# Optimization experiments

Measured on AMD Instinct MI355X. Metric: run time of the kernel, lower is better.

Reference implementation:

```python
import jax, jax.numpy as jnp
import numpy as np

B, S, D, H = 256, 64, 1024, 16
DH = D // H          # 64
BOARD = 8
NREL = 2 * (BOARD - 1) + 1  # 15


def _rel_indices():
    # Relative row/col offsets between all pairs of board squares, shifted to [0, 2*(BOARD-1)]
    coords = np.arange(S)
    row = coords // BOARD
    col = coords % BOARD
    rr = row[:, None] - row[None, :] + (BOARD - 1)  # (S, S)
    rc = col[:, None] - col[None, :] + (BOARD - 1)  # (S, S)
    return jnp.asarray(rr), jnp.asarray(rc)


def setup_inputs() -> dict:
    key = jax.random.key(0)
    ks = jax.random.split(key, 12)
    p = lambda k, sh: jax.random.normal(k, sh, jnp.float32) * 0.02
    return {
        "x": jax.random.normal(ks[0], (B, S, D), jnp.float32),
        "wq": p(ks[1], (D, D)),
        "wk": p(ks[2], (D, D)),
        "wv": p(ks[3], (D, D)),
        "wo": p(ks[4], (D, D)),
        "bo": jnp.zeros((D,), jnp.float32),
        "eq_h": p(ks[5], (NREL, DH)),
        "eq_w": p(ks[6], (NREL, DH)),
        "ek_h": p(ks[7], (NREL, DH)),
        "ek_w": p(ks[8], (NREL, DH)),
        "ev_h": p(ks[9], (NREL, DH)),
        "ev_w": p(ks[10], (NREL, DH)),
    }


def reference(x, wq, wk, wv, wo, bo, eq_h, eq_w, ek_h, ek_w, ev_h, ev_w):
    rr, rc = _rel_indices()
    rel_q = eq_h[rr] + eq_w[rc]  # (S, S, DH)
    rel_k = ek_h[rr] + ek_w[rc]
    rel_v = ev_h[rr] + ev_w[rc]

    def heads(y):
        return y.reshape(B, S, H, DH).transpose(0, 2, 1, 3)  # (B, H, S, DH)

    q = heads(x @ wq.T)
    k = heads(x @ wk.T)
    v = heads(x @ wv.T)

    # (q_i + rq_ij) . (k_j + rk_ij), expanded to avoid the (B,H,S,S,DH) intermediates
    scores = (
        jnp.einsum('bhid,bhjd->bhij', q, k)
        + jnp.einsum('bhid,ijd->bhij', q, rel_k)
        + jnp.einsum('ijd,bhjd->bhij', rel_q, k)
        + jnp.sum(rel_q * rel_k, axis=-1)[None, None]
    )
    attn = jax.nn.softmax(scores / jnp.sqrt(jnp.float32(DH)), axis=-1)  # (B, H, S, S)

    # sum_j attn_ij * (v_j + rv_ij)
    ctx = (
        jnp.einsum('bhij,bhjd->bhid', attn, v)
        + jnp.einsum('bhij,ijd->bhid', attn, rel_v)
    )
    ctx = ctx.transpose(0, 2, 1, 3).reshape(B, S, D)
    return ctx @ wo.T + bo
```

## Files before the change

kernel.cpp:

```cpp
#include <hip/hip_runtime.h>
#include <hip/hip_bf16.h>

typedef __hip_bfloat16 bf16;
typedef __attribute__((ext_vector_type(8))) short short8;
typedef __attribute__((ext_vector_type(8))) unsigned short ushort8;
typedef __attribute__((ext_vector_type(4))) float floatx4;

__device__ __forceinline__ short f2s(float x) {
  bf16 h = __float2bfloat16(x);
  short s;
  __builtin_memcpy(&s, &h, 2);
  return s;
}

__device__ __forceinline__ void gl_lds16(const bf16* g, bf16* l) {
  __builtin_amdgcn_global_load_lds(
      (const __attribute__((address_space(1))) unsigned int*)g,
      (__attribute__((address_space(3))) unsigned int*)l, 16, 0, 0);
}

#define MFMA16(a, b, c) __builtin_amdgcn_mfma_f32_16x16x32_bf16((a), (b), (c), 0, 0, 0)

__global__ __launch_bounds__(256) void convert_f32_bf16(
    const float* __restrict__ src, bf16* __restrict__ dst, int n) {
  const int i = (blockIdx.x * 256 + threadIdx.x) * 8;
  if (i + 7 < n) {
    float4 a = *(const float4*)(src + i);
    float4 b = *(const float4*)(src + i + 4);
    short8 r;
    r[0] = f2s(a.x); r[1] = f2s(a.y); r[2] = f2s(a.z); r[3] = f2s(a.w);
    r[4] = f2s(b.x); r[5] = f2s(b.y); r[6] = f2s(b.z); r[7] = f2s(b.w);
    *(short8*)(dst + i) = r;
  }
}

__global__ __launch_bounds__(256) void precompute_tables(
    const float* __restrict__ eqh, const float* __restrict__ eqw,
    const float* __restrict__ ekh, const float* __restrict__ ekw,
    const float* __restrict__ evh, const float* __restrict__ evw,
    bf16* __restrict__ ews, float* __restrict__ S4f)
{
  const int t = threadIdx.x;
  if (t < 96) {
    const int tb = t >> 4, row = t & 15;
    const float* src[6] = {eqh, eqw, ekh, ekw, evh, evw};
    bf16* dst = ews + tb * 1024 + row * 64;
    if (row < 15) {
      const float* s = src[tb] + row * 64;
      #pragma unroll
      for (int d = 0; d < 64; d += 8) {
        float4 a = *(const float4*)(s + d);
        float4 b2 = *(const float4*)(s + d + 4);
        short8 rr;
        rr[0] = f2s(a.x); rr[1] = f2s(a.y); rr[2] = f2s(a.z); rr[3] = f2s(a.w);
        rr[4] = f2s(b2.x); rr[5] = f2s(b2.y); rr[6] = f2s(b2.z); rr[7] = f2s(b2.w);
        *(short8*)(dst + d) = rr;
      }
    } else {
      const short8 z = {0, 0, 0, 0, 0, 0, 0, 0};
      #pragma unroll
      for (int d = 0; d < 64; d += 8) *(short8*)(dst + d) = z;
    }
  }
  if (t < 225) {
    const int r = t / 15, c = t % 15;
    float s = 0.f;
    for (int d = 0; d < 64; ++d)
      s += (eqh[r * 64 + d] + eqw[c * 64 + d]) * (ekh[r * 64 + d] + ekw[c * 64 + d]);
    S4f[t] = s;
  }
}

template <int TAG>
__global__ __launch_bounds__(256) void gemm_bt(
    const bf16* __restrict__ A,
    const void* __restrict__ W0, const void* __restrict__ W1, const void* __restrict__ W2,
    int wBf,
    const float* __restrict__ bias, int hasBias,
    bf16* __restrict__ O0, bf16* __restrict__ O1, bf16* __restrict__ O2,
    float* __restrict__ Ofp, int outF32)
{
  __shared__ bf16 As[128 * 64];
  __shared__ bf16 Bs[128 * 64];

  const int m0 = blockIdx.x * 128;
  const int by = blockIdx.y;
  const int which = by >> 3;
  const void* W = (which == 0) ? W0 : (which == 1) ? W1 : W2;
  bf16* O = (which == 0) ? O0 : (which == 1) ? O1 : O2;
  const int n0 = (by & 7) * 128;

  const int t = threadIdx.x;
  const int lane = t & 63, w = t >> 6;
  const int lrow = lane >> 3, lcol = (lane & 7) * 8;
  const int wm = w >> 1, wn = w & 1;
  const int quad = lane >> 4, n16 = lane & 15;

  const int swzA = ((lrow & 1) << 5) | (((lrow >> 1) & 3) << 3);
  const int gcol = lcol ^ swzA;
  const int swzR = ((n16 & 1) << 5) | (((n16 >> 1) & 3) << 3);

  floatx4 acc[4][4];
  const floatx4 zero4 = {0.f, 0.f, 0.f, 0.f};
  #pragma unroll
  for (int mi = 0; mi < 4; ++mi)
    #pragma unroll
    for (int ni = 0; ni < 4; ++ni) acc[mi][ni] = zero4;

  const int arowb = m0 + w * 32 + lrow;
  const int browb = n0 + w * 32 + lrow;
  bf16* lau = As + w * 2048;
  bf16* lbu = Bs + w * 2048;

  if (wBf) {
    const bf16* Wb = (const bf16*)W;
    for (int k0 = 0; k0 < 1024; k0 += 64) {
      if (k0) __syncthreads();
      const bf16* ga = A + arowb * 1024 + k0 + gcol;
      const bf16* gw = Wb + browb * 1024 + k0 + gcol;
      #pragma unroll
      for (int c = 0; c < 4; ++c) {
        gl_lds16(ga + c * 8192, lau + c * 512);
        gl_lds16(gw + c * 8192, lbu + c * 512);
      }
      __syncthreads();
      #pragma unroll
      for (int ks = 0; ks < 2; ++ks) {
        short8 af[4], bfv[4];
        #pragma unroll
        for (int mi = 0; mi < 4; ++mi)
          af[mi] = *(const short8*)(As + (wm * 64 + mi * 16 + n16) * 64 +
                                    ((ks * 32 + quad * 8) ^ swzR));
        #pragma unroll
        for (int ni = 0; ni < 4; ++ni)
          bfv[ni] = *(const short8*)(Bs + (wn * 64 + ni * 16 + n16) * 64 +
                                     ((ks * 32 + quad * 8) ^ swzR));
        #pragma unroll
        for (int mi = 0; mi < 4; ++mi)
          #pragma unroll
          for (int ni = 0; ni < 4; ++ni)
            acc[mi][ni] = MFMA16(af[mi], bfv[ni], acc[mi][ni]);
      }
    }
  } else {
    const float* Wf = (const float*)W;
    for (int k0 = 0; k0 < 1024; k0 += 64) {
      short8 rb[4];
      #pragma unroll
      for (int c = 0; c < 4; ++c) {
        const float* f = Wf + (browb + c * 8) * 1024 + k0 + gcol;
        float4 a = *(const float4*)f;
        float4 b = *(const float4*)(f + 4);
        short8 r;
        r[0] = f2s(a.x); r[1] = f2s(a.y); r[2] = f2s(a.z); r[3] = f2s(a.w);
        r[4] = f2s(b.x); r[5] = f2s(b.y); r[6] = f2s(b.z); r[7] = f2s(b.w);
        rb[c] = r;
      }
      if (k0) __syncthreads();
      const bf16* ga = A + arowb * 1024 + k0 + gcol;
      #pragma unroll
      for (int c = 0; c < 4; ++c) {
        gl_lds16(ga + c * 8192, lau + c * 512);
        *(short8*)(lbu + lane * 8 + c * 512) = rb[c];
      }
      __syncthreads();
      #pragma unroll
      for (int ks = 0; ks < 2; ++ks) {
        short8 af[4], bfv[4];
        #pragma unroll
        for (int mi = 0; mi < 4; ++mi)
          af[mi] = *(const short8*)(As + (wm * 64 + mi * 16 + n16) * 64 +
                                    ((ks * 32 + quad * 8) ^ swzR));
        #pragma unroll
        for (int ni = 0; ni < 4; ++ni)
          bfv[ni] = *(const short8*)(Bs + (wn * 64 + ni * 16 + n16) * 64 +
                                     ((ks * 32 + quad * 8) ^ swzR));
        #pragma unroll
        for (int mi = 0; mi < 4; ++mi)
          #pragma unroll
          for (int ni = 0; ni < 4; ++ni)
            acc[mi][ni] = MFMA16(af[mi], bfv[ni], acc[mi][ni]);
      }
    }
  }

  #pragma unroll
  for (int ni = 0; ni < 4; ++ni) {
    const int col = n0 + wn * 64 + ni * 16 + n16;
    const float bv = hasBias ? bias[col] : 0.f;
    #pragma unroll
    for (int mi = 0; mi < 4; ++mi) {
      #pragma unroll
      for (int r = 0; r < 4; ++r) {
        const int row = m0 + wm * 64 + mi * 16 + quad * 4 + r;
        if (outF32) Ofp[row * 1024 + col] = acc[mi][ni][r] + bv;
        else        O[row * 1024 + col] = __float2bfloat16(acc[mi][ni][r] + bv);
      }
    }
  }
}

__global__ __launch_bounds__(256, 3) void attn_rel(
    const bf16* __restrict__ Q, const bf16* __restrict__ Km, const bf16* __restrict__ V,
    const bf16* __restrict__ ews, const float* __restrict__ S4f,
    bf16* __restrict__ Ctx)
{
  __shared__ bf16 vT[64][106];
  __shared__ bf16 pa[64][104];
  __shared__ float Ahs[64][16], Aws[64][16];
  __shared__ float Bhs[15][64], Bws[15][64];
  __shared__ float S4s[225];

  const int t = threadIdx.x;
  const int b = blockIdx.x >> 4, h = blockIdx.x & 15;
  const int base = b * 65536 + h * 64;
  const int lane = t & 63, w = t >> 6;
  const int quad = lane >> 4, n16 = lane & 15;

  const bf16* qrow = Q + base + (w * 16 + n16) * 1024 + quad * 8;
  short8 aq0 = *(const short8*)(qrow);
  short8 aq1 = *(const short8*)(qrow + 32);
  short8 bk0[4], bk1[4];
  #pragma unroll
  for (int nj = 0; nj < 4; ++nj) {
    const bf16* krow = Km + base + (nj * 16 + n16) * 1024 + quad * 8;
    bk0[nj] = *(const short8*)(krow);
    bk1[nj] = *(const short8*)(krow + 32);
  }
  short8 ebf[4][2];
  #pragma unroll
  for (int tb = 0; tb < 4; ++tb) {
    const bf16* er = ews + tb * 1024 + n16 * 64 + quad * 8;
    ebf[tb][0] = *(const short8*)(er);
    ebf[tb][1] = *(const short8*)(er + 32);
  }

  {
    const int r = t >> 2, c0 = (t & 3) * 16;
    const bf16* vrow = V + base + r * 1024 + c0;
    int4 v0 = *(const int4*)(vrow);
    int4 v1 = *(const int4*)(vrow + 8);
    const unsigned short* p0 = (const unsigned short*)&v0;
    const unsigned short* p1 = (const unsigned short*)&v1;
    #pragma unroll
    for (int ii = 0; ii < 8; ++ii) {
      *(unsigned short*)&vT[c0 + ii][r] = p0[ii];
      *(unsigned short*)&vT[c0 + 8 + ii][r] = p1[ii];
    }
    if (t < 60) {
      const int r2 = t >> 2, d0 = (t & 3) * 16;
      ushort8 pe0 = *(const ushort8*)(ews + 4096 + r2 * 64 + d0);
      ushort8 pe1 = *(const ushort8*)(ews + 4096 + r2 * 64 + d0 + 8);
      ushort8 pf0 = *(const ushort8*)(ews + 5120 + r2 * 64 + d0);
      ushort8 pf1 = *(const ushort8*)(ews + 5120 + r2 * 64 + d0 + 8);
      #pragma unroll
      for (int ii = 0; ii < 8; ++ii) {
        *(unsigned short*)&vT[d0 + ii][64 + r2] = pe0[ii];
        *(unsigned short*)&vT[d0 + 8 + ii][64 + r2] = pe1[ii];
        *(unsigned short*)&vT[d0 + ii][79 + r2] = pf0[ii];
        *(unsigned short*)&vT[d0 + 8 + ii][79 + r2] = pf1[ii];
      }
    }
    if (t < 64) {
      *(unsigned short*)&vT[t][94] = 0; *(unsigned short*)&vT[t][95] = 0;
      *(unsigned short*)&pa[t][94] = 0; *(unsigned short*)&pa[t][95] = 0;
    }
    if (t < 225) S4s[t] = S4f[t];
  }

  floatx4 cqk[4];
  #pragma unroll
  for (int nj = 0; nj < 4; ++nj) {
    floatx4 c = {0.f, 0.f, 0.f, 0.f};
    c = MFMA16(aq0, bk0[nj], c);
    c = MFMA16(aq1, bk1[nj], c);
    cqk[nj] = c;
  }
  {
    floatx4 cah = {0.f, 0.f, 0.f, 0.f}, caw = cah, cbh = cah, cbw = cah;
    cah = MFMA16(aq0, ebf[2][0], cah); cah = MFMA16(aq1, ebf[2][1], cah);
    caw = MFMA16(aq0, ebf[3][0], caw); caw = MFMA16(aq1, ebf[3][1], caw);
    cbh = MFMA16(bk0[w], ebf[0][0], cbh); cbh = MFMA16(bk1[w], ebf[0][1], cbh);
    cbw = MFMA16(bk0[w], ebf[1][0], cbw); cbw = MFMA16(bk1[w], ebf[1][1], cbw);
    #pragma unroll
    for (int r = 0; r < 4; ++r) {
      const int i = w * 16 + quad * 4 + r;
      Ahs[i][n16] = cah[r];
      Aws[i][n16] = caw[r];
      if (n16 < 15) { Bhs[n16][i] = cbh[r]; Bws[n16][i] = cbw[r]; }
    }
  }
  __syncthreads();

  const int i_base = w * 16 + quad * 4;
  float xv[4][4];
  #pragma unroll
  for (int nj = 0; nj < 4; ++nj) {
    const int j = nj * 16 + n16;
    const int rowj = j >> 3, colj = j & 7;
    #pragma unroll
    for (int r = 0; r < 4; ++r) {
      const int i = i_base + r;
      const int rowi = i >> 3, coli = i & 7;
      const int rr = rowi - rowj + 7, rc = coli - colj + 7;
      xv[r][nj] = (cqk[nj][r] + Ahs[i][rr] + Aws[i][rc] + Bhs[rr][j] + Bws[rc][j]
                   + S4s[rr * 15 + rc]) * 0.125f;
    }
  }
  #pragma unroll
  for (int r = 0; r < 4; ++r) {
    const int i = i_base + r;
    const int rowi = i >> 3, coli = i & 7;
    float mx = fmaxf(fmaxf(xv[r][0], xv[r][1]), fmaxf(xv[r][2], xv[r][3]));
    #pragma unroll
    for (int off = 1; off < 16; off <<= 1) mx = fmaxf(mx, __shfl_xor(mx, off));
    float p[4];
    float sm = 0.f;
    #pragma unroll
    for (int nj = 0; nj < 4; ++nj) { p[nj] = __expf(xv[r][nj] - mx); sm += p[nj]; }
    #pragma unroll
    for (int off = 1; off < 16; off <<= 1) sm += __shfl_xor(sm, off);
    const float inv = 1.0f / sm;
    #pragma unroll
    for (int nj = 0; nj < 4; ++nj) {
      p[nj] *= inv;
      pa[i][nj * 16 + n16] = __float2bfloat16(p[nj]);
    }
    float ph[4];
    #pragma unroll
    for (int nj = 0; nj < 4; ++nj) {
      float v = p[nj];
      v += __shfl_xor(v, 1); v += __shfl_xor(v, 2); v += __shfl_xor(v, 4);
      ph[nj] = v;
    }
    float s4 = p[0] + p[1] + p[2] + p[3];
    float pw = s4 + __shfl_xor(s4, 8);
    if ((n16 & 7) == 0) {
      const int hh = n16 >> 3;
      #pragma unroll
      for (int nj = 0; nj < 4; ++nj) {
        const int g = nj * 2 + hh;
        pa[i][64 + rowi + 7 - g] = __float2bfloat16(ph[nj]);
      }
    } else if (n16 < 8) {
      const int z = n16 - 1;
      pa[i][64 + (z < rowi ? z : z + 8)] = __float2bfloat16(0.f);
    }
    if (n16 < 8) {
      pa[i][79 + coli + 7 - n16] = __float2bfloat16(pw);
    } else {
      const int z = n16 - 8;
      pa[i][79 + (z < coli ? z : z + 8)] = __float2bfloat16(0.f);
    }
  }
  __threadfence_block();

  short8 ap[3];
  #pragma unroll
  for (int ksb = 0; ksb < 3; ++ksb)
    ap[ksb] = *(const short8*)&pa[w * 16 + n16][ksb * 32 + quad * 8];
  #pragma unroll
  for (int nj = 0; nj < 4; ++nj) {
    floatx4 c = {0.f, 0.f, 0.f, 0.f};
    #pragma unroll
    for (int ksb = 0; ksb < 3; ++ksb) {
      short8 bv = *(const short8*)&vT[nj * 16 + n16][ksb * 32 + quad * 8];
      c = MFMA16(ap[ksb], bv, c);
    }
    #pragma unroll
    for (int r = 0; r < 4; ++r) {
      const int i = i_base + r;
      Ctx[base + i * 1024 + nj * 16 + n16] = __float2bfloat16(c[r]);
    }
  }
}

extern "C" void kernel_launch(void* const* d_in, const int* in_sizes, int n_in,
                              void* d_out, int out_size, void* d_ws, size_t ws_size,
                              hipStream_t stream) {
  const float* x   = (const float*)d_in[0];
  const float* wq  = (const float*)d_in[1];
  const float* wk  = (const float*)d_in[2];
  const float* wv  = (const float*)d_in[3];
  const float* wo  = (const float*)d_in[4];
  const float* bo  = (const float*)d_in[5];
  const float* eqh = (const float*)d_in[6];
  const float* eqw = (const float*)d_in[7];
  const float* ekh = (const float*)d_in[8];
  const float* ekw = (const float*)d_in[9];
  const float* evh = (const float*)d_in[10];
  const float* evw = (const float*)d_in[11];
  float* outf = (float*)d_out;

  const size_t hdr = (ws_size - 16384) & ~(size_t)1023;
  bf16* ewsB = (bf16*)((char*)d_ws + hdr);
  float* S4f = (float*)((char*)d_ws + hdr + 12288);
  precompute_tables<<<1, 256, 0, stream>>>(eqh, eqw, ekh, ekw, evh, evw, ewsB, S4f);

  if (ws_size >= (size_t)73 * 1024 * 1024) {
    bf16* qb = (bf16*)d_ws;
    bf16* kb = qb + 16777216;
    bf16* wqb = kb + 16777216;
    bf16* wkb = wqb + 1048576;
    bf16* wvb = wkb + 1048576;
    bf16* wob = wvb + 1048576;
    bf16* xb = (bf16*)d_out;
    bf16* vb = (bf16*)((char*)d_out + 33554432);

    convert_f32_bf16<<<8192, 256, 0, stream>>>(x, xb, 16777216);
    convert_f32_bf16<<<512, 256, 0, stream>>>(wq, wqb, 1048576);
    convert_f32_bf16<<<512, 256, 0, stream>>>(wk, wkb, 1048576);
    convert_f32_bf16<<<512, 256, 0, stream>>>(wv, wvb, 1048576);
    convert_f32_bf16<<<512, 256, 0, stream>>>(wo, wob, 1048576);

    gemm_bt<0><<<dim3(128, 24), 256, 0, stream>>>(
        xb, wqb, wkb, wvb, 1, nullptr, 0, qb, kb, vb, nullptr, 0);
    attn_rel<<<dim3(4096), 256, 0, stream>>>(qb, kb, vb, ewsB, S4f, qb);
    gemm_bt<1><<<dim3(128, 8), 256, 0, stream>>>(
        qb, wob, nullptr, nullptr, 1, bo, 1, nullptr, nullptr, nullptr, outf, 1);
  } else {
    bf16* xb0 = (bf16*)((char*)d_out + 16777216);
    bf16* xb1 = (bf16*)((char*)d_out + 50331648);
    bf16* vQ2 = (bf16*)((char*)d_out + 33554432);
    bf16* qb = (bf16*)d_ws;
    bf16* kb = qb + 8388608;
    const int fastW = (ws_size >= (size_t)42 * 1024 * 1024) ? 1 : 0;
    bf16* wqb = kb + 8388608;
    bf16* wkb = wqb + 1048576;
    bf16* wvb = wkb + 1048576;
    bf16* wob = wvb + 1048576;

    convert_f32_bf16<<<4096, 256, 0, stream>>>(x, xb0, 8388608);
    convert_f32_bf16<<<4096, 256, 0, stream>>>(x + 8388608, xb1, 8388608);
    if (fastW) {
      convert_f32_bf16<<<512, 256, 0, stream>>>(wq, wqb, 1048576);
      convert_f32_bf16<<<512, 256, 0, stream>>>(wk, wkb, 1048576);
      convert_f32_bf16<<<512, 256, 0, stream>>>(wv, wvb, 1048576);
      convert_f32_bf16<<<512, 256, 0, stream>>>(wo, wob, 1048576);
    }

    for (int hh = 0; hh < 2; ++hh) {
      const bf16* xh = hh ? xb1 : xb0;
      gemm_bt<0><<<dim3(64, 24), 256, 0, stream>>>(
          xh,
          fastW ? (const void*)wqb : (const void*)wq,
          fastW ? (const void*)wkb : (const void*)wk,
          fastW ? (const void*)wvb : (const void*)wv,
          fastW, nullptr, 0, qb, kb, vQ2, nullptr, 0);
      attn_rel<<<dim3(2048), 256, 0, stream>>>(qb, kb, vQ2, ewsB, S4f, qb);
      gemm_bt<1><<<dim3(64, 8), 256, 0, stream>>>(
          qb,
          fastW ? (const void*)wob : (const void*)wo, nullptr, nullptr,
          fastW, bo, 1, nullptr, nullptr, nullptr,
          outf + (size_t)hh * 8388608, 1);
    }
  }
}
```

Measured before the change: 386.4 us.

## Replace projection GEMMs with 256x256-tile, 4-stage pipelined 512-thread kernel

Adds a new gemm256 kernel with 256x256 output tiles, 512 threads, a 4-deep LDS ring filled by direct global-to-LDS loads with explicit vmcnt waits, swizzled LDS layout, an XCD-aware block remap and s_setprio around the MFMA bursts. It replaces gemm_bt for the QKV and output projections wherever bf16 weights are available. The goal is more operand reuse per tile and memory latency hidden behind MFMA work. In exchange it uses 128KB of LDS and many accumulator registers, which limits occupancy and makes the hand-written wait counts fragile.

Result: slower. 394.2 us (+2.0%).

```diff
diff --git a/kernel.cpp b/kernel.cpp
--- a/kernel.cpp
+++ b/kernel.cpp
@@ -20,6 +20,14 @@
 }
 
 #define MFMA16(a, b, c) __builtin_amdgcn_mfma_f32_16x16x32_bf16((a), (b), (c), 0, 0, 0)
+
+__device__ __forceinline__ void bar() {
+  asm volatile("" ::: "memory");
+  __builtin_amdgcn_s_barrier();
+  asm volatile("" ::: "memory");
+}
+
+#define VMCNT(N) asm volatile("s_waitcnt vmcnt(" #N ")" ::: "memory")
 
 __global__ __launch_bounds__(256) void convert_f32_bf16(
     const float* __restrict__ src, bf16* __restrict__ dst, int n) {
@@ -68,6 +76,130 @@
     for (int d = 0; d < 64; ++d)
       s += (eqh[r * 64 + d] + eqw[c * 64 + d]) * (ekh[r * 64 + d] + ekw[c * 64 + d]);
     S4f[t] = s;
+  }
+}
+
+template <int TAG>
+__global__ __launch_bounds__(512, 2) void gemm256(
+    const bf16* __restrict__ A,
+    const bf16* __restrict__ W0, const bf16* __restrict__ W1, const bf16* __restrict__ W2,
+    const float* __restrict__ bias, int hasBias,
+    bf16* __restrict__ O0, bf16* __restrict__ O1, bf16* __restrict__ O2,
+    float* __restrict__ Ofp, int outF32)
+{
+  __shared__ bf16 lds[65536];
+
+  const int nx = gridDim.x;
+  const int nwg = nx * gridDim.y;
+  const int orig = blockIdx.y * nx + blockIdx.x;
+  const int id = (orig & 7) * (nwg >> 3) + (orig >> 3);
+  const int bx = id % nx;
+  const int by = id / nx;
+
+  const int m0 = bx * 256;
+  const int which = by >> 2;
+  const bf16* W = (which == 0) ? W0 : (which == 1) ? W1 : W2;
+  bf16* O = (which == 0) ? O0 : (which == 1) ? O1 : O2;
+  const int n0 = (by & 3) * 256;
+
+  const int t = threadIdx.x;
+  const int lane = t & 63, w = t >> 6;
+  const int wm = w >> 2, wn = w & 3;
+  const int quad = lane >> 4, n16 = lane & 15;
+
+  const int srow = (t >> 6) * 16 + ((t & 63) >> 2);
+  const int scol = ((t & 3) * 8) ^ (((t >> 5) & 1) << 4);
+  const bf16* Abase = A + (m0 + srow) * 1024 + scol;
+  const bf16* Bbase = W + (n0 + srow) * 1024 + scol;
+  const int wdst = w * 512;
+
+  const int swzq = (quad * 8) ^ ((n16 >> 3) << 4);
+  const int aoff = wm * 4096 + n16 * 32 + swzq;
+  const int boff = wn * 2048 + n16 * 32 + swzq;
+
+  floatx4 acc[8][4];
+  const floatx4 zero4 = {0.f, 0.f, 0.f, 0.f};
+  #pragma unroll
+  for (int mi = 0; mi < 8; ++mi)
+    #pragma unroll
+    for (int ni = 0; ni < 4; ++ni) acc[mi][ni] = zero4;
+
+  #pragma unroll
+  for (int p = 0; p < 3; ++p) {
+    const bf16* ga = Abase + p * 32;
+    bf16* la = lds + p * 16384 + wdst;
+    gl_lds16(ga, la); gl_lds16(ga + 131072, la + 4096);
+    const bf16* gb = Bbase + p * 32;
+    bf16* lb = lds + p * 16384 + 8192 + wdst;
+    gl_lds16(gb, lb); gl_lds16(gb + 131072, lb + 4096);
+  }
+  VMCNT(8);
+  bar();
+
+#define TILE_STEP(TT, DOSTAGE, WAITSEQ) do {                                   \
+    const bf16* bA_ = lds + ((TT) & 3) * 16384;                                \
+    const bf16* bB_ = bA_ + 8192;                                              \
+    short8 af_[4], bq_[4];                                                     \
+    _Pragma("unroll")                                                          \
+    for (int mi = 0; mi < 4; ++mi)                                             \
+      af_[mi] = *(const short8*)(bA_ + aoff + mi * 512);                       \
+    _Pragma("unroll")                                                          \
+    for (int ni = 0; ni < 4; ++ni)                                             \
+      bq_[ni] = *(const short8*)(bB_ + boff + ni * 512);                       \
+    if (DOSTAGE) {                                                             \
+      const bf16* g_ = Abase + ((TT) + 3) * 32;                                \
+      bf16* l_ = lds + (((TT) + 3) & 3) * 16384 + wdst;                        \
+      gl_lds16(g_, l_); gl_lds16(g_ + 131072, l_ + 4096);                      \
+    }                                                                          \
+    bar();                                                                     \
+    __builtin_amdgcn_s_setprio(1);                                             \
+    _Pragma("unroll")                                                          \
+    for (int mi = 0; mi < 4; ++mi)                                             \
+      _Pragma("unroll")                                                        \
+      for (int ni = 0; ni < 4; ++ni)                                           \
+        acc[mi][ni] = MFMA16(af_[mi], bq_[ni], acc[mi][ni]);                   \
+    __builtin_amdgcn_s_setprio(0);                                             \
+    _Pragma("unroll")                                                          \
+    for (int mi = 0; mi < 4; ++mi)                                             \
+      af_[mi] = *(const short8*)(bA_ + aoff + 2048 + mi * 512);                \
+    if (DOSTAGE) {                                                             \
+      const bf16* g_ = Bbase + ((TT) + 3) * 32;                                \
+      bf16* l_ = lds + (((TT) + 3) & 3) * 16384 + 8192 + wdst;                 \
+      gl_lds16(g_, l_); gl_lds16(g_ + 131072, l_ + 4096);                      \
+    }                                                                          \
+    bar();                                                                     \
+    __builtin_amdgcn_s_setprio(1);                                             \
+    _Pragma("unroll")                                                          \
+    for (int mi = 0; mi < 4; ++mi)                                             \
+      _Pragma("unroll")                                                        \
+      for (int ni = 0; ni < 4; ++ni)                                           \
+        acc[mi + 4][ni] = MFMA16(af_[mi], bq_[ni], acc[mi + 4][ni]);           \
+    __builtin_amdgcn_s_setprio(0);                                             \
+    WAITSEQ;                                                                   \
+  } while (0)
+
+  #pragma unroll 1
+  for (int tt = 0; tt < 29; ++tt) {
+    TILE_STEP(tt, 1, VMCNT(8); bar());
+  }
+  TILE_STEP(29, 0, VMCNT(4); bar());
+  TILE_STEP(30, 0, VMCNT(0); bar());
+  TILE_STEP(31, 0, (void)0);
+#undef TILE_STEP
+
+  #pragma unroll
+  for (int ni = 0; ni < 4; ++ni) {
+    const int col = n0 + wn * 64 + ni * 16 + n16;
+    const float bv = hasBias ? bias[col] : 0.f;
+    #pragma unroll
+    for (int mi = 0; mi < 8; ++mi) {
+      #pragma unroll
+      for (int r = 0; r < 4; ++r) {
+        const int row = m0 + wm * 128 + mi * 16 + quad * 4 + r;
+        if (outF32) Ofp[row * 1024 + col] = acc[mi][ni][r] + bv;
+        else        O[row * 1024 + col] = __float2bfloat16(acc[mi][ni][r] + bv);
+      }
+    }
   }
 }
 
@@ -413,11 +545,11 @@
     convert_f32_bf16<<<512, 256, 0, stream>>>(wv, wvb, 1048576);
     convert_f32_bf16<<<512, 256, 0, stream>>>(wo, wob, 1048576);
 
-    gemm_bt<0><<<dim3(128, 24), 256, 0, stream>>>(
-        xb, wqb, wkb, wvb, 1, nullptr, 0, qb, kb, vb, nullptr, 0);
+    gemm256<0><<<dim3(64, 12), 512, 0, stream>>>(
+        xb, wqb, wkb, wvb, nullptr, 0, qb, kb, vb, nullptr, 0);
     attn_rel<<<dim3(4096), 256, 0, stream>>>(qb, kb, vb, ewsB, S4f, qb);
-    gemm_bt<1><<<dim3(128, 8), 256, 0, stream>>>(
-        qb, wob, nullptr, nullptr, 1, bo, 1, nullptr, nullptr, nullptr, outf, 1);
+    gemm256<1><<<dim3(64, 4), 512, 0, stream>>>(
+        qb, wob, nullptr, nullptr, bo, 1, nullptr, nullptr, nullptr, outf, 1);
   } else {
     bf16* xb0 = (bf16*)((char*)d_out + 16777216);
     bf16* xb1 = (bf16*)((char*)d_out + 50331648);
@@ -441,18 +573,25 @@
 
     for (int hh = 0; hh < 2; ++hh) {
       const bf16* xh = hh ? xb1 : xb0;
-      gemm_bt<0><<<dim3(64, 24), 256, 0, stream>>>(
-          xh,
-          fastW ? (const void*)wqb : (const void*)wq,
-          fastW ? (const void*)wkb : (const void*)wk,
-          fastW ? (const void*)wvb : (const void*)wv,
-          fastW, nullptr, 0, qb, kb, vQ2, nullptr, 0);
+      if (fastW) {
+        gemm256<0><<<dim3(32, 12), 512, 0, stream>>>(
+            xh, wqb, wkb, wvb, nullptr, 0, qb, kb, vQ2, nullptr, 0);
+      } else {
+        gemm_bt<0><<<dim3(64, 24), 256, 0, stream>>>(
+            xh, (const void*)wq, (const void*)wk, (const void*)wv,
+            0, nullptr, 0, qb, kb, vQ2, nullptr, 0);
+      }
       attn_rel<<<dim3(2048), 256, 0, stream>>>(qb, kb, vQ2, ewsB, S4f, qb);
-      gemm_bt<1><<<dim3(64, 8), 256, 0, stream>>>(
-          qb,
-          fastW ? (const void*)wob : (const void*)wo, nullptr, nullptr,
-          fastW, bo, 1, nullptr, nullptr, nullptr,
-          outf + (size_t)hh * 8388608, 1);
-    }
-  }
-}
+      if (fastW) {
+        gemm256<1><<<dim3(32, 4), 512, 0, stream>>>(
+            qb, wob, nullptr, nullptr, bo, 1, nullptr, nullptr, nullptr,
+            outf + (size_t)hh * 8388608, 1);
+      } else {
+        gemm_bt<1><<<dim3(64, 8), 256, 0, stream>>>(
+            qb, (const void*)wo, nullptr, nullptr,
+            0, bo, 1, nullptr, nullptr, nullptr,
+            outf + (size_t)hh * 8388608, 1);
+      }
+    }
+  }
+}
```
